# Performance work log

Hardware: AMD Instinct MI355X
Metric: run time of the kernel (lower is better)

## Reference

```python
import jax, jax.numpy as jnp
import numpy as np
from jax import lax

B, L, E = 2, 2048, 1024          # batch, seq_len, embed_dim
NL = 2                            # n_layers
DI = 2 * E                        # d_inner (expand=2)
DS = 16                           # d_state
DC = 4                            # d_conv
DTR = (E + 15) // 16              # dt_rank = ceil(d_model/16) = 64


def setup_inputs() -> dict:
    key = jax.random.key(0)
    ks = jax.random.split(key, 12)
    s = 0.02
    inp = {
        "x": jax.random.normal(ks[0], (B, L, E), jnp.float32),
        "pos_embed": jax.random.normal(ks[1], (L, E), jnp.float32) * s,
        "in_proj_w": jax.random.normal(ks[2], (NL, 2 * DI, E), jnp.float32) * s,
        "conv_w": jax.random.normal(ks[3], (NL, DI, DC), jnp.float32) * s,
        "conv_b": jnp.zeros((NL, DI), jnp.float32),
        "x_proj_w": jax.random.normal(ks[4], (NL, DTR + 2 * DS, DI), jnp.float32) * s,
        "dt_proj_w": jax.random.normal(ks[5], (NL, DI, DTR), jnp.float32) * s,
        "dt_bias": jax.random.normal(ks[6], (NL, DI), jnp.float32) * 0.1,
        "A_log": jnp.broadcast_to(jnp.log(jnp.arange(1, DS + 1, dtype=jnp.float32)), (NL, DI, DS)) + 0.0,
        "D_skip": jnp.ones((NL, DI), jnp.float32),
        "out_proj_w": jax.random.normal(ks[7], (NL, E, DI), jnp.float32) * s,
        "norm_w": jnp.ones((NL, E), jnp.float32),
    }
    return inp


def _rmsnorm(x, w, eps=1e-6):
    return x * lax.rsqrt(jnp.mean(x * x, axis=-1, keepdims=True) + eps) * w


def _mamba(h, in_w, cw, cb, xw, dtw, dtb, A_log, Dp, ow):
    # h: (B, L, E)
    xz = jnp.einsum("ble,de->bld", h, in_w)          # (B, L, 2*DI)
    xc, z = jnp.split(xz, 2, axis=-1)                 # each (B, L, DI)
    # causal depthwise conv1d (kernel DC)
    xp = jnp.pad(xc, ((0, 0), (DC - 1, 0), (0, 0)))
    xconv = cb
    acc = jnp.zeros_like(xc)
    for k in range(DC):
        acc = acc + cw[:, k] * xp[:, k:k + xc.shape[1], :]
    xc = jax.nn.silu(acc + cb)
    # input-dependent SSM params
    x_dbl = jnp.einsum("bld,rd->blr", xc, xw)         # (B, L, DTR+2*DS)
    dt, Bm, C = jnp.split(x_dbl, [DTR, DTR + DS], axis=-1)
    delta = jax.nn.softplus(jnp.einsum("blr,dr->bld", dt, dtw) + dtb)  # (B, L, DI)
    A = -jnp.exp(A_log)                               # (DI, DS)

    def step(hst, inp):
        d, bm, c, u = inp                             # (B,DI),(B,DS),(B,DS),(B,DI)
        hst = jnp.exp(d[..., None] * A) * hst + (d * u)[..., None] * bm[:, None, :]
        y = jnp.einsum("bdn,bn->bd", hst, c)
        return hst, y

    h0 = jnp.zeros((h.shape[0], DI, DS), h.dtype)
    _, ys = lax.scan(step, h0, (delta.swapaxes(0, 1), Bm.swapaxes(0, 1),
                                C.swapaxes(0, 1), xc.swapaxes(0, 1)))
    y = ys.swapaxes(0, 1) + xc * Dp                   # (B, L, DI)
    y = y * jax.nn.silu(z)
    return jnp.einsum("bld,ed->ble", y, ow)


def reference(x, pos_embed, in_proj_w, conv_w, conv_b, x_proj_w, dt_proj_w,
              dt_bias, A_log, D_skip, out_proj_w, norm_w):
    h = x + pos_embed[None, :x.shape[1]]
    for i in range(in_proj_w.shape[0]):
        y = _mamba(h, in_proj_w[i], conv_w[i], conv_b[i], x_proj_w[i],
                   dt_proj_w[i], dt_bias[i], A_log[i], D_skip[i], out_proj_w[i])
        h = _rmsnorm(y + h, norm_w[i])
    return h
```

## Files before the change

### kernel.cpp

```cpp
#include <hip/hip_runtime.h>

#define B_   2
#define L_   2048
#define E_   1024
#define NL_  2
#define DI_  2048
#define DS_  16
#define DC_  4
#define DTR_ 64
#define NXD_ 96
#define M_   (B_ * L_)
#define NCH_ 64
#define LC_  32

typedef __attribute__((ext_vector_type(8))) short bf16x8;
typedef __attribute__((ext_vector_type(4))) float f32x4;

__device__ __forceinline__ float bf2f(unsigned short u) {
    return __uint_as_float(((unsigned)u) << 16);
}
__device__ __forceinline__ unsigned short f2bf(float f) {
    unsigned u = __float_as_uint(f);
    u += 0x7fff + ((u >> 16) & 1);
    return (unsigned short)(u >> 16);
}

#define LOG2E_ 1.44269504f
#define LN2_   0.69314718f

__device__ __forceinline__ float sigmoidf_(float x) {
    return __builtin_amdgcn_rcpf(1.f + __builtin_amdgcn_exp2f(-x * LOG2E_));
}
__device__ __forceinline__ float softplusf_(float x) {
    float e = __builtin_amdgcn_exp2f(x * LOG2E_);
    float s = LN2_ * __builtin_amdgcn_logf(1.f + e);
    return x > 15.f ? x : s;
}
__device__ __forceinline__ float expf_(float x) {
    return __builtin_amdgcn_exp2f(x * LOG2E_);
}
__device__ __forceinline__ float ldin(const void* p, size_t i, int isbf) {
    return isbf ? bf2f(((const unsigned short*)p)[i]) : ((const float*)p)[i];
}
__device__ __forceinline__ void gld_lds16(const unsigned short* g, unsigned short* l) {
    __builtin_amdgcn_global_load_lds(
        (const __attribute__((address_space(1))) unsigned int*)g,
        (__attribute__((address_space(3))) unsigned int*)l, 16, 0, 0);
}
__device__ __forceinline__ bf16x8 ds_read128_(unsigned byteoff) {
    bf16x8 r;
    asm volatile("ds_read_b128 %0, %1" : "=&v"(r) : "v"(byteoff));
    return r;
}

__device__ __forceinline__ void expvec(int fast, float dv, const float* a2, float* e) {
    if (fast) {
        float p1 = __builtin_amdgcn_exp2f(dv * a2[0]);
        float p2 = p1 * p1, p4 = p2 * p2, p8 = p4 * p4;
        e[0] = p1;        e[1] = p2;        e[2] = p2 * p1;   e[3] = p4;
        e[4] = p4 * p1;   e[5] = p4 * p2;   e[6] = e[5] * p1; e[7] = p8;
        e[8] = p8 * p1;   e[9] = p8 * p2;   e[10] = e[9] * p1; e[11] = p8 * p4;
        e[12] = e[11] * p1; e[13] = e[11] * p2; e[14] = e[13] * p1; e[15] = p8 * p8;
    } else {
#pragma unroll
        for (int n = 0; n < 16; ++n) e[n] = __builtin_amdgcn_exp2f(dv * a2[n]);
    }
}

__global__ __launch_bounds__(256) void detect_kernel(const unsigned* __restrict__ x,
                                                     int* __restrict__ flags)
{
    __shared__ int cnt;
    if (threadIdx.x == 0) cnt = 0;
    __syncthreads();
    unsigned v = x[threadIdx.x];
    int e = (v >> 7) & 0xFF;
    if (e >= 90 && e <= 140) atomicAdd(&cnt, 1);
    __syncthreads();
    if (threadIdx.x == 0) {
        flags[0] = (cnt >= 192) ? 1 : 0;
        flags[1] = 1;
        flags[2] = 1;
    }
}

__global__ __launch_bounds__(256) void chk_alog(
    const void* __restrict__ alog, int* __restrict__ flags)
{
    int isbf = flags[0];
    int i = blockIdx.x * 256 + threadIdx.x;
    int layer = i / (DI_ * DS_);
    int n = i & (DS_ - 1);
    float a  = -expf_(ldin(alog, i, isbf));
    float a0 = -expf_(ldin(alog, i - n, isbf));
    float want = (n + 1) * a0;
    if (fabsf(a - want) > 0.02f * fabsf(want))
        atomicAnd(&flags[1 + layer], 0);
}

#define WB_IN_  0
#define WB_XW_  4194304
#define WB_DTW_ 4456448
#define WB_OW_  4587520
#define WB_TOT_ 6684672
__global__ __launch_bounds__(256) void cvt_layer_kernel(
    const void* __restrict__ inw, const void* __restrict__ xw,
    const void* __restrict__ dtw, const void* __restrict__ ow,
    int layer, unsigned short* __restrict__ wbuf, const int* __restrict__ flag)
{
    int isbf = *flag;
    int i = blockIdx.x * 256 + threadIdx.x;
    if (isbf && (i < WB_XW_ || i >= WB_DTW_)) return;
    unsigned short v;
    if (i < WB_XW_) {
        v = isbf ? ((const unsigned short*)inw)[(size_t)layer * 2 * DI_ * E_ + i]
                 : f2bf(((const float*)inw)[(size_t)layer * 2 * DI_ * E_ + i]);
    } else if (i < WB_DTW_) {
        int j = i - WB_XW_; int r = j >> 11, k = j & (DI_ - 1);
        v = (r < NXD_)
          ? (isbf ? ((const unsigned short*)xw)[(size_t)layer * NXD_ * DI_ + (size_t)r * DI_ + k]
                  : f2bf(((const float*)xw)[(size_t)layer * NXD_ * DI_ + (size_t)r * DI_ + k]))
          : (unsigned short)0;
    } else if (i < WB_OW_) {
        int j = i - WB_DTW_;
        v = isbf ? ((const unsigned short*)dtw)[(size_t)layer * DI_ * DTR_ + j]
                 : f2bf(((const float*)dtw)[(size_t)layer * DI_ * DTR_ + j]);
    } else {
        int j = i - WB_OW_;
        v = isbf ? ((const unsigned short*)ow)[(size_t)layer * E_ * DI_ + j]
                 : f2bf(((const float*)ow)[(size_t)layer * E_ * DI_ + j]);
    }
    wbuf[i] = v;
}

__global__ __launch_bounds__(256) void add_pos_kernel(
    const void* __restrict__ x, const void* __restrict__ pos,
    float* __restrict__ h, unsigned short* __restrict__ h16,
    const int* __restrict__ flag)
{
    int isbf = *flag;
    int i = blockIdx.x * 256 + threadIdx.x;
    float v = ldin(x, i, isbf) + ldin(pos, i & (L_ * E_ - 1), isbf);
    h[i] = v;
    h16[i] = f2bf(v);
}

__global__ __launch_bounds__(256) void gemm_mfma(
    const unsigned short* __restrict__ A, int lda,
    const unsigned short* __restrict__ W, int ldw,
    void* __restrict__ C, int ldc, int Ksplit, size_t cSliceStride,
    const void* __restrict__ bias, size_t boff,
    void* __restrict__ C2, int ep, const int* __restrict__ flag,
    const unsigned short* __restrict__ Worig)
{
    __shared__ unsigned short As[128 * 64];
    __shared__ unsigned short Bs[128 * 64];
    int isbf = flag ? *flag : 1;
    const unsigned short* Wp = (Worig && isbf) ? Worig : W;
    int tid = threadIdx.x;
    int lane = tid & 63, w = tid >> 6;
    int m0 = blockIdx.x * 128, n0 = blockIdx.y * 128;
    int wm = (w >> 1) * 64, wn = (w & 1) * 64;
    int col = lane & 15, quad = lane >> 4;
    int kstart = blockIdx.z * Ksplit;

    f32x4 acc[4][4];
#pragma unroll
    for (int i = 0; i < 4; ++i)
#pragma unroll
        for (int j = 0; j < 4; ++j)
            acc[i][j] = (f32x4){0.f, 0.f, 0.f, 0.f};

    for (int kt = kstart; kt < kstart + Ksplit; kt += 64) {
#pragma unroll
        for (int i = 0; i < 4; ++i) {
            int seg = i * 4 + w;
            int q = seg * 64 + lane;
            int r = q >> 3, cd = q & 7;
            int cs = cd ^ (r & 7);
            gld_lds16(A + (size_t)(m0 + r) * lda + kt + cs * 8, &As[seg * 512]);
            gld_lds16(Wp + (size_t)(n0 + r) * ldw + kt + cs * 8, &Bs[seg * 512]);
        }
        __syncthreads();
#pragma unroll
        for (int ks = 0; ks < 2; ++ks) {
            bf16x8 af[4], bfr[4];
#pragma unroll
            for (int t = 0; t < 4; ++t) {
                int rowA = wm + t * 16 + col;
                int ca = ks * 4 + quad;
                af[t]  = *(const bf16x8*)&As[rowA * 64 + ((ca ^ (rowA & 7)) * 8)];
                int rowB = wn + t * 16 + col;
                bfr[t] = *(const bf16x8*)&Bs[rowB * 64 + ((ca ^ (rowB & 7)) * 8)];
            }
#pragma unroll
            for (int tm = 0; tm < 4; ++tm)
#pragma unroll
                for (int tn = 0; tn < 4; ++tn)
                    acc[tm][tn] = __builtin_amdgcn_mfma_f32_16x16x32_bf16(
                        af[tm], bfr[tn], acc[tm][tn], 0, 0, 0);
        }
        __syncthreads();
    }

    float* Cp = (float*)C + (size_t)blockIdx.z * cSliceStride;
#pragma unroll
    for (int tm = 0; tm < 4; ++tm)
#pragma unroll
        for (int tn = 0; tn < 4; ++tn)
#pragma unroll
            for (int rg = 0; rg < 4; ++rg) {
                int gm = m0 + wm + tm * 16 + quad * 4 + rg;
                int gn = n0 + wn + tn * 16 + col;
                float v = acc[tm][tn][rg];
                if (ep == 0) {
                    Cp[(size_t)gm * ldc + gn] = v;
                } else {
                    v = softplusf_(v + ldin(bias, boff + gn, isbf));
                    ((unsigned short*)C)[(size_t)gm * ldc + gn] = f2bf(v);
                }
            }
}

template <int KS, int MH, int RB, int CHK>
__device__ __forceinline__ void g8_phase(
    unsigned baseA, unsigned baseB,
    bf16x8 (&af)[4], bf16x8 (&bfr)[4], f32x4 (&acc)[8][4],
    int doStage, int st_t, int st_isB, int st_ks,
    const unsigned short* srcA, const unsigned short* srcW,
    unsigned short* ldsb, int w)
{
    if (RB) {
#pragma unroll
        for (int j = 0; j < 4; ++j)
            bfr[j] = ds_read128_(baseB + j * 2048 + KS * 1024);
    }
#pragma unroll
    for (int f = 0; f < 4; ++f)
        af[f] = ds_read128_(baseA + MH * 8192 + f * 2048 + KS * 1024);
    if (doStage) {
        const unsigned short* s0 = (st_isB ? srcW : srcA)
            + (size_t)w * 16 * E_ + st_t * 64 + st_ks * 32;
        unsigned short* d0 = ldsb + (st_t & 1) * 32768 + st_isB * 16384
            + w * 1024 + st_ks * 512;
        gld_lds16(s0, d0);
        gld_lds16(s0 + (size_t)8 * 16 * E_, d0 + 8 * 1024);
    }
    __builtin_amdgcn_s_barrier();
    asm volatile("s_waitcnt lgkmcnt(0)" ::: "memory");
    __builtin_amdgcn_sched_barrier(0);
    __builtin_amdgcn_s_setprio(1);
#pragma unroll
    for (int f = 0; f < 4; ++f)
#pragma unroll
        for (int j = 0; j < 4; ++j)
            acc[MH * 4 + f][j] = __builtin_amdgcn_mfma_f32_16x16x32_bf16(
                af[f], bfr[j], acc[MH * 4 + f][j], 0, 0, 0);
    __builtin_amdgcn_s_setprio(0);
    if (CHK == 8) { asm volatile("s_waitcnt vmcnt(8)" ::: "memory"); __builtin_amdgcn_sched_barrier(0); }
    if (CHK == 4) { asm volatile("s_waitcnt vmcnt(4)" ::: "memory"); __builtin_amdgcn_sched_barrier(0); }
    if (CHK == 0) { asm volatile("s_waitcnt vmcnt(0)"  ::: "memory"); __builtin_amdgcn_sched_barrier(0); }
    __builtin_amdgcn_s_barrier();
}

__global__ __launch_bounds__(512) void gemm_inproj8(
    const unsigned short* __restrict__ A,
    const unsigned short* __restrict__ Wbuf,
    const unsigned short* __restrict__ Worig,
    const int* __restrict__ flag,
    unsigned short* __restrict__ Cx,
    unsigned short* __restrict__ Cz)
{
    __shared__ unsigned short lds[65536];
    const unsigned short* W = (*flag) ? Worig : Wbuf;
    int tid = threadIdx.x;
    int lane = tid & 63, w = tid >> 6;
    int wr = w >> 2, wc = w & 3;
    int col = lane & 15, quad = lane >> 4;

    int flat = blockIdx.y * 16 + blockIdx.x;
    int nn = (flat & 7) * 32 + (flat >> 3);
    int cch = nn >> 5, wi = nn & 31;
    int bx = (cch & 3) * 4 + (wi & 3);
    int by = (cch >> 2) * 8 + (wi >> 2);
    int m0 = bx * 256, n0 = by * 256;

    const unsigned short* srcA = A + (size_t)(m0 + (lane & 15)) * E_ + (lane >> 4) * 8;
    const unsigned short* srcW = W + (size_t)(n0 + (lane & 15)) * E_ + (lane >> 4) * 8;

    unsigned baseA0 = (unsigned)(wr * 8 * 2048 + quad * 256 + col * 16);
    unsigned baseB0 = (unsigned)(32768 + wc * 4 * 2048 + quad * 256 + col * 16);
    unsigned baseA1 = baseA0 + 65536, baseB1 = baseB0 + 65536;

    f32x4 acc[8][4];
#pragma unroll
    for (int i = 0; i < 8; ++i)
#pragma unroll
        for (int j = 0; j < 4; ++j)
            acc[i][j] = (f32x4){0.f, 0.f, 0.f, 0.f};
    bf16x8 af[4], bfr[4];

#define G8STAGE(t_, isB_, ks_) { \
    const unsigned short* s0 = ((isB_) ? srcW : srcA) + (size_t)w * 16 * E_ + (t_) * 64 + (ks_) * 32; \
    unsigned short* d0 = lds + ((t_) & 1) * 32768 + (isB_) * 16384 + w * 1024 + (ks_) * 512; \
    gld_lds16(s0, d0); gld_lds16(s0 + (size_t)8 * 16 * E_, d0 + 8 * 1024); }

    G8STAGE(0, 0, 0) G8STAGE(0, 1, 0) G8STAGE(0, 0, 1) G8STAGE(0, 1, 1)
    G8STAGE(1, 0, 0) G8STAGE(1, 1, 0)
    asm volatile("s_waitcnt vmcnt(8)" ::: "memory");
    __builtin_amdgcn_sched_barrier(0);
    __builtin_amdgcn_s_barrier();

    for (int i = 0; i < 7; ++i) {
        int t1 = 2 * i + 1, t2 = 2 * i + 2, t3 = 2 * i + 3;
        g8_phase<0,0,1,-1>(baseA0, baseB0, af, bfr, acc, 1, t1, 0, 1, srcA, srcW, lds, w);
        g8_phase<0,1,0, 8>(baseA0, baseB0, af, bfr, acc, 1, t1, 1, 1, srcA, srcW, lds, w);
        g8_phase<1,0,1,-1>(baseA0, baseB0, af, bfr, acc, 1, t2, 0, 0, srcA, srcW, lds, w);
        g8_phase<1,1,0, 8>(baseA0, baseB0, af, bfr, acc, 1, t2, 1, 0, srcA, srcW, lds, w);
        g8_phase<0,0,1,-1>(baseA1, baseB1, af, bfr, acc, 1, t2, 0, 1, srcA, srcW, lds, w);
        g8_phase<0,1,0, 8>(baseA1, baseB1, af, bfr, acc, 1, t2, 1, 1, srcA, srcW, lds, w);
        g8_phase<1,0,1,-1>(baseA1, baseB1, af, bfr, acc, 1, t3, 0, 0, srcA, srcW, lds, w);
        g8_phase<1,1,0, 8>(baseA1, baseB1, af, bfr, acc, 1, t3, 1, 0, srcA, srcW, lds, w);
    }
    g8_phase<0,0,1,-1>(baseA0, baseB0, af, bfr, acc, 1, 15, 0, 1, srcA, srcW, lds, w);
    g8_phase<0,1,0, 8>(baseA0, baseB0, af, bfr, acc, 1, 15, 1, 1, srcA, srcW, lds, w);
    g8_phase<1,0,1,-1>(baseA0, baseB0, af, bfr, acc, 0, 0, 0, 0, srcA, srcW, lds, w);
    g8_phase<1,1,0, 4>(baseA0, baseB0, af, bfr, acc, 0, 0, 0, 0, srcA, srcW, lds, w);
    g8_phase<0,0,1,-1>(baseA1, baseB1, af, bfr, acc, 0, 0, 0, 0, srcA, srcW, lds, w);
    g8_phase<0,1,0, 0>(baseA1, baseB1, af, bfr, acc, 0, 0, 0, 0, srcA, srcW, lds, w);
    g8_phase<1,0,1,-1>(baseA1, baseB1, af, bfr, acc, 0, 0, 0, 0, srcA, srcW, lds, w);
    g8_phase<1,1,0,-1>(baseA1, baseB1, af, bfr, acc, 0, 0, 0, 0, srcA, srcW, lds, w);

    unsigned short* dst = (n0 < DI_) ? Cx : Cz;
    int nb = (n0 < DI_) ? n0 : n0 - DI_;
#pragma unroll
    for (int tm = 0; tm < 8; ++tm)
#pragma unroll
        for (int tn = 0; tn < 4; ++tn)
#pragma unroll
            for (int rg = 0; rg < 4; ++rg) {
                int gm = m0 + wr * 128 + tm * 16 + quad * 4 + rg;
                int gn = nb + wc * 64 + tn * 16 + col;
                dst[(size_t)gm * DI_ + gn] = f2bf(acc[tm][tn][rg]);
            }
#undef G8STAGE
}

__global__ __launch_bounds__(256) void xproj_reduce(
    const float* __restrict__ part, float* __restrict__ xdbl,
    unsigned short* __restrict__ dt16)
{
    int i = blockIdx.x * 256 + threadIdx.x;
    int r = i >> 7, c = i & 127;
    float v = 0.f;
#pragma unroll
    for (int s = 0; s < 8; ++s) v += part[(size_t)s * (M_ * 128) + i];
    if (c < NXD_) xdbl[(size_t)r * NXD_ + c] = v;
    if (c < DTR_) dt16[(size_t)r * DTR_ + c] = f2bf(v);
}

__global__ __launch_bounds__(256) void conv_prep(
    const void* __restrict__ cw, size_t cwoff, const void* __restrict__ cb,
    size_t cboff, float* __restrict__ cwT, float* __restrict__ cbF,
    const int* __restrict__ flag)
{
    int isbf = *flag;
    int d = blockIdx.x * 256 + threadIdx.x;
#pragma unroll
    for (int k = 0; k < DC_; ++k)
        cwT[k * DI_ + d] = ldin(cw, cwoff + (size_t)d * DC_ + k, isbf);
    cbF[d] = ldin(cb, cboff + d, isbf);
}

#define CT_ 4
__global__ __launch_bounds__(256) void conv_silu_v(
    const unsigned short* __restrict__ xcr16, const float* __restrict__ cwT,
    const float* __restrict__ cbF, unsigned short* __restrict__ xc16)
{
    int g = blockIdx.x;
    int bl0 = g * CT_;
    int l0 = bl0 & (L_ - 1);
    int d = threadIdx.x * 8;

    float w[DC_][8], bias[8];
#pragma unroll
    for (int k = 0; k < DC_; ++k) {
        *(float4*)&w[k][0] = *(const float4*)&cwT[k * DI_ + d];
        *(float4*)&w[k][4] = *(const float4*)&cwT[k * DI_ + d + 4];
    }
    *(float4*)&bias[0] = *(const float4*)&cbF[d];
    *(float4*)&bias[4] = *(const float4*)&cbF[d + 4];

    float xr[DC_ - 1 + CT_][8];
#pragma unroll
    for (int r = 0; r < DC_ - 1 + CT_; ++r) {
        int l = l0 - (DC_ - 1) + r;
        if (l >= 0) {
            bf16x8 v = *(const bf16x8*)&xcr16[(size_t)(bl0 - (DC_ - 1) + r) * DI_ + d];
#pragma unroll
            for (int j = 0; j < 8; ++j) xr[r][j] = bf2f((unsigned short)v[j]);
        } else {
#pragma unroll
            for (int j = 0; j < 8; ++j) xr[r][j] = 0.f;
        }
    }

#pragma unroll
    for (int t = 0; t < CT_; ++t) {
        float acc[8];
#pragma unroll
        for (int j = 0; j < 8; ++j) acc[j] = bias[j];
#pragma unroll
        for (int k = 0; k < DC_; ++k)
#pragma unroll
            for (int j = 0; j < 8; ++j)
                acc[j] = fmaf(w[k][j], xr[t + k][j], acc[j]);
        bf16x8 ov;
#pragma unroll
        for (int j = 0; j < 8; ++j) {
            float s = acc[j] * sigmoidf_(acc[j]);
            ov[j] = (short)f2bf(s);
        }
        *(bf16x8*)&xc16[(size_t)(bl0 + t) * DI_ + d] = ov;
    }
}

__global__ __launch_bounds__(256) void scan_part1(
    const unsigned short* __restrict__ dl16, const unsigned short* __restrict__ xc16,
    const float* __restrict__ xdbl,
    const void* __restrict__ A_log, size_t aoff,
    float* __restrict__ sumdbuf, float* __restrict__ scrS,
    const int* __restrict__ flags, int layer)
{
    int isbf = flags[0], fast = flags[1 + layer];
    __shared__ float bs[LC_][16];
    int c = blockIdx.y;
    int b = blockIdx.x >> 3;
    int d = ((blockIdx.x & 7) << 8) + threadIdx.x;
    for (int i = threadIdx.x; i < LC_ * 16; i += 256) {
        int l = i >> 4, n = i & 15;
        bs[l][n] = xdbl[((size_t)b * L_ + c * LC_ + l) * NXD_ + DTR_ + n];
    }
    __syncthreads();
    float a2[16];
#pragma unroll
    for (int n = 0; n < 16; ++n)
        a2[n] = -expf_(ldin(A_log, aoff + (size_t)d * DS_ + n, isbf)) * LOG2E_;
    float s[16] = {};
    float sumd = 0.f;
    const unsigned short* dp = dl16 + ((size_t)b * L_ + c * LC_) * DI_ + d;
    const unsigned short* up = xc16 + ((size_t)b * L_ + c * LC_) * DI_ + d;
    for (int l0 = 0; l0 < LC_; l0 += 4) {
        float dvv[4], uv[4];
#pragma unroll
        for (int q = 0; q < 4; ++q) {
            dvv[q] = bf2f(dp[(size_t)(l0 + q) * DI_]);
            uv[q]  = bf2f(up[(size_t)(l0 + q) * DI_]);
        }
#pragma unroll
        for (int q = 0; q < 4; ++q) {
            int l = l0 + q;
            float dv = dvv[q];
            sumd += dv;
            float dvu = dv * uv[q];
            float e[16];
            expvec(fast, dv, a2, e);
            float4 b0 = *(const float4*)&bs[l][0];
            float4 b1 = *(const float4*)&bs[l][4];
            float4 b2 = *(const float4*)&bs[l][8];
            float4 b3 = *(const float4*)&bs[l][12];
            float bv[16] = {b0.x,b0.y,b0.z,b0.w, b1.x,b1.y,b1.z,b1.w,
                            b2.x,b2.y,b2.z,b2.w, b3.x,b3.y,b3.z,b3.w};
#pragma unroll
            for (int n = 0; n < 16; ++n)
                s[n] = fmaf(e[n], s[n], dvu * bv[n]);
        }
    }
    int g = b * DI_ + d;
    sumdbuf[(size_t)c * (B_ * DI_) + g] = sumd;
    size_t base = ((size_t)c * (B_ * DI_) + g) * 16;
#pragma unroll
    for (int q = 0; q < 4; ++q)
        *(float4*)&scrS[base + q * 4] =
            make_float4(s[q*4], s[q*4+1], s[q*4+2], s[q*4+3]);
}

__global__ __launch_bounds__(256) void scan_combine(
    const float* __restrict__ sumdbuf, float* __restrict__ scrS,
    const void* __restrict__ A_log, size_t aoff, const int* __restrict__ flags)
{
    int isbf = flags[0];
    int t = blockIdx.x * 256 + threadIdx.x;
    int g = t >> 4, n = t & 15;
    int d = g & (DI_ - 1);
    float a2 = -expf_(ldin(A_log, aoff + (size_t)d * DS_ + n, isbf)) * LOG2E_;
    float sd[NCH_], sl[NCH_];
#pragma unroll
    for (int c = 0; c < NCH_; ++c) {
        sd[c] = sumdbuf[(size_t)c * (B_ * DI_) + g];
        sl[c] = scrS[(size_t)c * (B_ * DI_ * 16) + t];
    }
    float s = 0.f;
#pragma unroll
    for (int c = 0; c < NCH_; ++c) {
        float P = __builtin_amdgcn_exp2f(a2 * sd[c]);
        float nxt = fmaf(P, s, sl[c]);
        scrS[(size_t)c * (B_ * DI_ * 16) + t] = s;
        s = nxt;
    }
}

__global__ __launch_bounds__(256) void scan_part2(
    const unsigned short* __restrict__ dl16, unsigned short* __restrict__ xc16,
    const float* __restrict__ xdbl, const unsigned short* __restrict__ z,
    const void* __restrict__ A_log, size_t aoff,
    const void* __restrict__ Dskip, size_t doff,
    const float* __restrict__ scrS, const int* __restrict__ flags, int layer)
{
    int isbf = flags[0], fast = flags[1 + layer];
    __shared__ float bs[LC_][32];
    int c = blockIdx.y;
    int b = blockIdx.x >> 3;
    int d = ((blockIdx.x & 7) << 8) + threadIdx.x;
    for (int i = threadIdx.x; i < LC_ * 32; i += 256) {
        int l = i >> 5, n = i & 31;
        bs[l][n] = xdbl[((size_t)b * L_ + c * LC_ + l) * NXD_ + DTR_ + n];
    }
    __syncthreads();
    float a2[16];
#pragma unroll
    for (int n = 0; n < 16; ++n)
        a2[n] = -expf_(ldin(A_log, aoff + (size_t)d * DS_ + n, isbf)) * LOG2E_;
    float Dv = ldin(Dskip, doff + d, isbf);
    int g = b * DI_ + d;
    size_t sbase = ((size_t)c * (B_ * DI_) + g) * 16;
    float s[16];
#pragma unroll
    for (int q = 0; q < 4; ++q) {
        float4 sv = *(const float4*)&scrS[sbase + q * 4];
        s[q*4] = sv.x; s[q*4+1] = sv.y; s[q*4+2] = sv.z; s[q*4+3] = sv.w;
    }

    const unsigned short* dp = dl16 + ((size_t)b * L_ + c * LC_) * DI_ + d;
    unsigned short* up = xc16 + ((size_t)b * L_ + c * LC_) * DI_ + d;
    const unsigned short* zp = z + ((size_t)b * L_ + c * LC_) * DI_ + d;
    for (int l0 = 0; l0 < LC_; l0 += 4) {
        float dvv[4], uv[4], zv[4];
#pragma unroll
        for (int q = 0; q < 4; ++q) {
            dvv[q] = bf2f(dp[(size_t)(l0 + q) * DI_]);
            uv[q]  = bf2f(up[(size_t)(l0 + q) * DI_]);
            zv[q]  = bf2f(zp[(size_t)(l0 + q) * DI_]);
        }
#pragma unroll
        for (int q = 0; q < 4; ++q) {
            int l = l0 + q;
            float dv = dvv[q], u = uv[q];
            float dvu = dv * u;
            float e[16];
            expvec(fast, dv, a2, e);
            float4 b0 = *(const float4*)&bs[l][0];
            float4 b1 = *(const float4*)&bs[l][4];
            float4 b2 = *(const float4*)&bs[l][8];
            float4 b3 = *(const float4*)&bs[l][12];
            float4 c0 = *(const float4*)&bs[l][16];
            float4 c1 = *(const float4*)&bs[l][20];
            float4 c2 = *(const float4*)&bs[l][24];
            float4 c3 = *(const float4*)&bs[l][28];
            float bv[16] = {b0.x,b0.y,b0.z,b0.w, b1.x,b1.y,b1.z,b1.w,
                            b2.x,b2.y,b2.z,b2.w, b3.x,b3.y,b3.z,b3.w};
            float cv[16] = {c0.x,c0.y,c0.z,c0.w, c1.x,c1.y,c1.z,c1.w,
                            c2.x,c2.y,c2.z,c2.w, c3.x,c3.y,c3.z,c3.w};
            float y = 0.f;
#pragma unroll
            for (int n = 0; n < 16; ++n) {
                s[n] = fmaf(e[n], s[n], dvu * bv[n]);
                y = fmaf(s[n], cv[n], y);
            }
            float zvv = zv[q];
            up[(size_t)l * DI_] = f2bf((y + u * Dv) * (zvv * sigmoidf_(zvv)));
        }
    }
}

__global__ __launch_bounds__(256) void rmsnorm_kernel(
    const float* __restrict__ y0, const float* __restrict__ y1,
    float* __restrict__ h, unsigned short* __restrict__ h16,
    const void* __restrict__ nw, size_t nwoff, void* __restrict__ out,
    int write_out, const int* __restrict__ flag)
{
    int isbf = *flag;
    __shared__ float red[4];
    int row = blockIdx.x;
    float* hp = h + (size_t)row * E_;
    float v[4]; float ss = 0.f;
#pragma unroll
    for (int i = 0; i < 4; ++i) {
        int e = threadIdx.x + i * 256;
        size_t idx = (size_t)row * E_ + e;
        v[i] = y0[idx] + y1[idx] + hp[e];
        ss += v[i] * v[i];
    }
#pragma unroll
    for (int off = 1; off < 64; off <<= 1) ss += __shfl_xor(ss, off, 64);
    if ((threadIdx.x & 63) == 0) red[threadIdx.x >> 6] = ss;
    __syncthreads();
    ss = red[0] + red[1] + red[2] + red[3];
    float scale = rsqrtf(ss * (1.f / E_) + 1e-6f);
#pragma unroll
    for (int i = 0; i < 4; ++i) {
        int e = threadIdx.x + i * 256;
        float hv = v[i] * scale * ldin(nw, nwoff + e, isbf);
        hp[e] = hv;
        h16[(size_t)row * E_ + e] = f2bf(hv);
        if (write_out) {
            size_t oi = (size_t)row * E_ + e;
            if (isbf) ((unsigned short*)out)[oi] = f2bf(hv);
            else      ((float*)out)[oi] = hv;
        }
    }
}

extern "C" void kernel_launch(void* const* d_in, const int* in_sizes, int n_in,
                              void* d_out, int out_size, void* d_ws, size_t ws_size,
                              hipStream_t stream)
{
    const void* x    = d_in[0];
    const void* pos  = d_in[1];
    const void* inw  = d_in[2];
    const void* cw   = d_in[3];
    const void* cb   = d_in[4];
    const void* xw   = d_in[5];
    const void* dtw  = d_in[6];
    const void* dtb  = d_in[7];
    const void* alog = d_in[8];
    const void* dsk  = d_in[9];
    const void* ow   = d_in[10];
    const void* nw   = d_in[11];

    float* ws = (float*)d_ws;
    float* h      = ws;
    unsigned short* h16  = (unsigned short*)(ws + 4194304);
    unsigned short* z16  = (unsigned short*)(ws + 6291456);
    unsigned short* xc16 = (unsigned short*)(ws + 10485760);
    float* D      = ws + 14680064;
    float* R      = ws + 23068672;
    float* xdbl   = ws + 27262976;
    unsigned short* dt16 = (unsigned short*)(ws + 27656192);
    float* sumd   = ws + 27787264;
    unsigned short* wbuf = (unsigned short*)(ws + 28049408);
    int* flags    = (int*)(ws + 31391744);

    unsigned short* xcr16 = (unsigned short*)R;
    float* xp_part = R;
    float* scrS    = R;
    unsigned short* dl16 = (unsigned short*)D;
    float* yout0 = D;
    float* yout1 = D + (size_t)M_ * E_;
    float* cwT = sumd;
    float* cbF = sumd + DC_ * DI_;

    detect_kernel<<<1, 256, 0, stream>>>((const unsigned*)x, flags);
    chk_alog<<<NL_ * DI_ * DS_ / 256, 256, 0, stream>>>(alog, flags);
    add_pos_kernel<<<M_ * E_ / 256, 256, 0, stream>>>(x, pos, h, h16, flags);

    for (int layer = 0; layer < NL_; ++layer) {
        const unsigned short* inws = (const unsigned short*)inw + (size_t)layer * 2 * DI_ * E_;
        const unsigned short* dtws = (const unsigned short*)dtw + (size_t)layer * DI_ * DTR_;
        const unsigned short* ows  = (const unsigned short*)ow  + (size_t)layer * E_ * DI_;

        cvt_layer_kernel<<<WB_TOT_ / 256, 256, 0, stream>>>(
            inw, xw, dtw, ow, layer, wbuf, flags);
        conv_prep<<<DI_ / 256, 256, 0, stream>>>(
            cw, (size_t)layer * DI_ * DC_, cb, (size_t)layer * DI_, cwT, cbF, flags);

        gemm_inproj8<<<dim3(M_ / 256, 2 * DI_ / 256, 1), 512, 0, stream>>>(
            h16, wbuf + WB_IN_, inws, flags, xcr16, z16);
        conv_silu_v<<<M_ / CT_, 256, 0, stream>>>(xcr16, cwT, cbF, xc16);
        gemm_mfma<<<dim3(M_ / 128, 1, 8), 256, 0, stream>>>(
            xc16, DI_, wbuf + WB_XW_, DI_, xp_part, 128, DI_ / 8, (size_t)M_ * 128,
            nullptr, 0, nullptr, 0, flags, nullptr);
        xproj_reduce<<<M_ * 128 / 256, 256, 0, stream>>>(xp_part, xdbl, dt16);
        gemm_mfma<<<dim3(M_ / 128, DI_ / 128, 1), 256, 0, stream>>>(
            dt16, DTR_, wbuf + WB_DTW_, DTR_, dl16, DI_, DTR_, 0,
            dtb, (size_t)layer * DI_, nullptr, 2, flags, dtws);
        scan_part1<<<dim3(B_ * DI_ / 256, NCH_), 256, 0, stream>>>(
            dl16, xc16, xdbl, alog, (size_t)layer * DI_ * DS_, sumd, scrS, flags, layer);
        scan_combine<<<B_ * DI_ * DS_ / 256, 256, 0, stream>>>(
            sumd, scrS, alog, (size_t)layer * DI_ * DS_, flags);
        scan_part2<<<dim3(B_ * DI_ / 256, NCH_), 256, 0, stream>>>(
            dl16, xc16, xdbl, z16, alog, (size_t)layer * DI_ * DS_,
            dsk, (size_t)layer * DI_, scrS, flags, layer);
        gemm_mfma<<<dim3(M_ / 128, E_ / 128, 2), 256, 0, stream>>>(
            xc16, DI_, wbuf + WB_OW_, DI_, yout0, E_, DI_ / 2, (size_t)M_ * E_,
            nullptr, 0, nullptr, 0, flags, ows);
        rmsnorm_kernel<<<M_, 256, 0, stream>>>(
            yout0, yout1, h, h16, nw, (size_t)layer * E_, d_out,
            layer == NL_ - 1 ? 1 : 0, flags);
    }
}
```

Before: 553.0 us.

## Software-pipeline scan loads, merge conv prep into cvt kernel, widen add_pos

Both scan passes now double-buffer their per-timestep loads of delta, u and z, issuing the next group of four loads before computing the current group. The goal is to hide global-memory latency in these serial recurrences. The conv weight and bias prep moves into the first blocks of the weight-conversion kernel, which saves one launch per layer. add_pos now does four elements per thread with a quarter of the blocks. Holding two load buffers adds register pressure in the scan kernels.

New measurement: 1.134 ms. 2.05x slower.

```diff
diff --git a/kernel.cpp b/kernel.cpp
--- a/kernel.cpp
+++ b/kernel.cpp
@@ -106,9 +106,18 @@
 __global__ __launch_bounds__(256) void cvt_layer_kernel(
     const void* __restrict__ inw, const void* __restrict__ xw,
     const void* __restrict__ dtw, const void* __restrict__ ow,
-    int layer, unsigned short* __restrict__ wbuf, const int* __restrict__ flag)
+    int layer, unsigned short* __restrict__ wbuf, const int* __restrict__ flag,
+    const void* __restrict__ cw, size_t cwoff, const void* __restrict__ cb,
+    size_t cboff, float* __restrict__ cwT, float* __restrict__ cbF)
 {
     int isbf = *flag;
+    if (blockIdx.x < DI_ / 256) {
+        int d = blockIdx.x * 256 + threadIdx.x;
+#pragma unroll
+        for (int k = 0; k < DC_; ++k)
+            cwT[k * DI_ + d] = ldin(cw, cwoff + (size_t)d * DC_ + k, isbf);
+        cbF[d] = ldin(cb, cboff + d, isbf);
+    }
     int i = blockIdx.x * 256 + threadIdx.x;
     if (isbf && (i < WB_XW_ || i >= WB_DTW_)) return;
     unsigned short v;
@@ -139,10 +148,14 @@
     const int* __restrict__ flag)
 {
     int isbf = *flag;
-    int i = blockIdx.x * 256 + threadIdx.x;
-    float v = ldin(x, i, isbf) + ldin(pos, i & (L_ * E_ - 1), isbf);
-    h[i] = v;
-    h16[i] = f2bf(v);
+    int i4 = (blockIdx.x * 256 + threadIdx.x) * 4;
+#pragma unroll
+    for (int q = 0; q < 4; ++q) {
+        int i = i4 + q;
+        float v = ldin(x, i, isbf) + ldin(pos, i & (L_ * E_ - 1), isbf);
+        h[i] = v;
+        h16[i] = f2bf(v);
+    }
 }
 
 __global__ __launch_bounds__(256) void gemm_mfma(
@@ -359,19 +372,6 @@
     if (c < DTR_) dt16[(size_t)r * DTR_ + c] = f2bf(v);
 }
 
-__global__ __launch_bounds__(256) void conv_prep(
-    const void* __restrict__ cw, size_t cwoff, const void* __restrict__ cb,
-    size_t cboff, float* __restrict__ cwT, float* __restrict__ cbF,
-    const int* __restrict__ flag)
-{
-    int isbf = *flag;
-    int d = blockIdx.x * 256 + threadIdx.x;
-#pragma unroll
-    for (int k = 0; k < DC_; ++k)
-        cwT[k * DI_ + d] = ldin(cw, cwoff + (size_t)d * DC_ + k, isbf);
-    cbF[d] = ldin(cb, cboff + d, isbf);
-}
-
 #define CT_ 4
 __global__ __launch_bounds__(256) void conv_silu_v(
     const unsigned short* __restrict__ xcr16, const float* __restrict__ cwT,
@@ -422,6 +422,84 @@
             ov[j] = (short)f2bf(s);
         }
         *(bf16x8*)&xc16[(size_t)(bl0 + t) * DI_ + d] = ov;
+    }
+}
+
+__device__ __forceinline__ void scan_ld2(const unsigned short* dp,
+    const unsigned short* up, int l0, float (&dvv)[4], float (&uv)[4])
+{
+#pragma unroll
+    for (int q = 0; q < 4; ++q) {
+        dvv[q] = bf2f(dp[(size_t)(l0 + q) * DI_]);
+        uv[q]  = bf2f(up[(size_t)(l0 + q) * DI_]);
+    }
+}
+__device__ __forceinline__ void scan_ld3(const unsigned short* dp,
+    const unsigned short* up, const unsigned short* zp, int l0,
+    float (&dvv)[4], float (&uv)[4], float (&zv)[4])
+{
+#pragma unroll
+    for (int q = 0; q < 4; ++q) {
+        dvv[q] = bf2f(dp[(size_t)(l0 + q) * DI_]);
+        uv[q]  = bf2f(up[(size_t)(l0 + q) * DI_]);
+        zv[q]  = bf2f(zp[(size_t)(l0 + q) * DI_]);
+    }
+}
+__device__ __forceinline__ void scan1_grp(int fast, const float* a2,
+    float (&s)[16], float& sumd, const float (&dvv)[4], const float (&uv)[4],
+    const float (*bs)[16], int l0)
+{
+#pragma unroll
+    for (int q = 0; q < 4; ++q) {
+        int l = l0 + q;
+        float dv = dvv[q];
+        sumd += dv;
+        float dvu = dv * uv[q];
+        float e[16];
+        expvec(fast, dv, a2, e);
+        float4 b0 = *(const float4*)&bs[l][0];
+        float4 b1 = *(const float4*)&bs[l][4];
+        float4 b2 = *(const float4*)&bs[l][8];
+        float4 b3 = *(const float4*)&bs[l][12];
+        float bv[16] = {b0.x,b0.y,b0.z,b0.w, b1.x,b1.y,b1.z,b1.w,
+                        b2.x,b2.y,b2.z,b2.w, b3.x,b3.y,b3.z,b3.w};
+#pragma unroll
+        for (int n = 0; n < 16; ++n)
+            s[n] = fmaf(e[n], s[n], dvu * bv[n]);
+    }
+}
+__device__ __forceinline__ void scan2_grp(int fast, const float* a2,
+    float (&s)[16], float Dv, const float (&dvv)[4], const float (&uv)[4],
+    const float (&zv)[4], const float (*bs)[32], int l0,
+    unsigned short* up)
+{
+#pragma unroll
+    for (int q = 0; q < 4; ++q) {
+        int l = l0 + q;
+        float dv = dvv[q], u = uv[q];
+        float dvu = dv * u;
+        float e[16];
+        expvec(fast, dv, a2, e);
+        float4 b0 = *(const float4*)&bs[l][0];
+        float4 b1 = *(const float4*)&bs[l][4];
+        float4 b2 = *(const float4*)&bs[l][8];
+        float4 b3 = *(const float4*)&bs[l][12];
+        float4 c0 = *(const float4*)&bs[l][16];
+        float4 c1 = *(const float4*)&bs[l][20];
+        float4 c2 = *(const float4*)&bs[l][24];
+        float4 c3 = *(const float4*)&bs[l][28];
+        float bv[16] = {b0.x,b0.y,b0.z,b0.w, b1.x,b1.y,b1.z,b1.w,
+                        b2.x,b2.y,b2.z,b2.w, b3.x,b3.y,b3.z,b3.w};
+        float cv[16] = {c0.x,c0.y,c0.z,c0.w, c1.x,c1.y,c1.z,c1.w,
+                        c2.x,c2.y,c2.z,c2.w, c3.x,c3.y,c3.z,c3.w};
+        float y = 0.f;
+#pragma unroll
+        for (int n = 0; n < 16; ++n) {
+            s[n] = fmaf(e[n], s[n], dvu * bv[n]);
+            y = fmaf(s[n], cv[n], y);
+        }
+        float zvv = zv[q];
+        up[(size_t)l * DI_] = f2bf((y + u * Dv) * (zvv * sigmoidf_(zvv)));
     }
 }
 
@@ -450,32 +528,20 @@
     float sumd = 0.f;
     const unsigned short* dp = dl16 + ((size_t)b * L_ + c * LC_) * DI_ + d;
     const unsigned short* up = xc16 + ((size_t)b * L_ + c * LC_) * DI_ + d;
-    for (int l0 = 0; l0 < LC_; l0 += 4) {
-        float dvv[4], uv[4];
-#pragma unroll
-        for (int q = 0; q < 4; ++q) {
-            dvv[q] = bf2f(dp[(size_t)(l0 + q) * DI_]);
-            uv[q]  = bf2f(up[(size_t)(l0 + q) * DI_]);
-        }
-#pragma unroll
-        for (int q = 0; q < 4; ++q) {
-            int l = l0 + q;
-            float dv = dvv[q];
-            sumd += dv;
-            float dvu = dv * uv[q];
-            float e[16];
-            expvec(fast, dv, a2, e);
-            float4 b0 = *(const float4*)&bs[l][0];
-            float4 b1 = *(const float4*)&bs[l][4];
-            float4 b2 = *(const float4*)&bs[l][8];
-            float4 b3 = *(const float4*)&bs[l][12];
-            float bv[16] = {b0.x,b0.y,b0.z,b0.w, b1.x,b1.y,b1.z,b1.w,
-                            b2.x,b2.y,b2.z,b2.w, b3.x,b3.y,b3.z,b3.w};
-#pragma unroll
-            for (int n = 0; n < 16; ++n)
-                s[n] = fmaf(e[n], s[n], dvu * bv[n]);
-        }
-    }
+
+    float dA[4], uA[4], dB[4], uB[4];
+    scan_ld2(dp, up, 0, dA, uA);
+#pragma unroll
+    for (int l0 = 0; l0 < LC_ - 8; l0 += 8) {
+        scan_ld2(dp, up, l0 + 4, dB, uB);
+        scan1_grp(fast, a2, s, sumd, dA, uA, bs, l0);
+        scan_ld2(dp, up, l0 + 8, dA, uA);
+        scan1_grp(fast, a2, s, sumd, dB, uB, bs, l0 + 4);
+    }
+    scan_ld2(dp, up, LC_ - 4, dB, uB);
+    scan1_grp(fast, a2, s, sumd, dA, uA, bs, LC_ - 8);
+    scan1_grp(fast, a2, s, sumd, dB, uB, bs, LC_ - 4);
+
     int g = b * DI_ + d;
     sumdbuf[(size_t)c * (B_ * DI_) + g] = sumd;
     size_t base = ((size_t)c * (B_ * DI_) + g) * 16;
@@ -544,43 +610,19 @@
     const unsigned short* dp = dl16 + ((size_t)b * L_ + c * LC_) * DI_ + d;
     unsigned short* up = xc16 + ((size_t)b * L_ + c * LC_) * DI_ + d;
     const unsigned short* zp = z + ((size_t)b * L_ + c * LC_) * DI_ + d;
-    for (int l0 = 0; l0 < LC_; l0 += 4) {
-        float dvv[4], uv[4], zv[4];
-#pragma unroll
-        for (int q = 0; q < 4; ++q) {
-            dvv[q] = bf2f(dp[(size_t)(l0 + q) * DI_]);
-            uv[q]  = bf2f(up[(size_t)(l0 + q) * DI_]);
-            zv[q]  = bf2f(zp[(size_t)(l0 + q) * DI_]);
-        }
-#pragma unroll
-        for (int q = 0; q < 4; ++q) {
-            int l = l0 + q;
-            float dv = dvv[q], u = uv[q];
-            float dvu = dv * u;
-            float e[16];
-            expvec(fast, dv, a2, e);
-            float4 b0 = *(const float4*)&bs[l][0];
-            float4 b1 = *(const float4*)&bs[l][4];
-            float4 b2 = *(const float4*)&bs[l][8];
-            float4 b3 = *(const float4*)&bs[l][12];
-            float4 c0 = *(const float4*)&bs[l][16];
-            float4 c1 = *(const float4*)&bs[l][20];
-            float4 c2 = *(const float4*)&bs[l][24];
-            float4 c3 = *(const float4*)&bs[l][28];
-            float bv[16] = {b0.x,b0.y,b0.z,b0.w, b1.x,b1.y,b1.z,b1.w,
-                            b2.x,b2.y,b2.z,b2.w, b3.x,b3.y,b3.z,b3.w};
-            float cv[16] = {c0.x,c0.y,c0.z,c0.w, c1.x,c1.y,c1.z,c1.w,
-                            c2.x,c2.y,c2.z,c2.w, c3.x,c3.y,c3.z,c3.w};
-            float y = 0.f;
-#pragma unroll
-            for (int n = 0; n < 16; ++n) {
-                s[n] = fmaf(e[n], s[n], dvu * bv[n]);
-                y = fmaf(s[n], cv[n], y);
-            }
-            float zvv = zv[q];
-            up[(size_t)l * DI_] = f2bf((y + u * Dv) * (zvv * sigmoidf_(zvv)));
-        }
-    }
+
+    float dA[4], uA[4], zA[4], dB[4], uB[4], zB[4];
+    scan_ld3(dp, up, zp, 0, dA, uA, zA);
+#pragma unroll
+    for (int l0 = 0; l0 < LC_ - 8; l0 += 8) {
+        scan_ld3(dp, up, zp, l0 + 4, dB, uB, zB);
+        scan2_grp(fast, a2, s, Dv, dA, uA, zA, bs, l0, up);
+        scan_ld3(dp, up, zp, l0 + 8, dA, uA, zA);
+        scan2_grp(fast, a2, s, Dv, dB, uB, zB, bs, l0 + 4, up);
+    }
+    scan_ld3(dp, up, zp, LC_ - 4, dB, uB, zB);
+    scan2_grp(fast, a2, s, Dv, dA, uA, zA, bs, LC_ - 8, up);
+    scan2_grp(fast, a2, s, Dv, dB, uB, zB, bs, LC_ - 4, up);
 }
 
 __global__ __launch_bounds__(256) void rmsnorm_kernel(
@@ -662,7 +704,7 @@
 
     detect_kernel<<<1, 256, 0, stream>>>((const unsigned*)x, flags);
     chk_alog<<<NL_ * DI_ * DS_ / 256, 256, 0, stream>>>(alog, flags);
-    add_pos_kernel<<<M_ * E_ / 256, 256, 0, stream>>>(x, pos, h, h16, flags);
+    add_pos_kernel<<<M_ * E_ / 1024, 256, 0, stream>>>(x, pos, h, h16, flags);
 
     for (int layer = 0; layer < NL_; ++layer) {
         const unsigned short* inws = (const unsigned short*)inw + (size_t)layer * 2 * DI_ * E_;
@@ -670,9 +712,8 @@
         const unsigned short* ows  = (const unsigned short*)ow  + (size_t)layer * E_ * DI_;
 
         cvt_layer_kernel<<<WB_TOT_ / 256, 256, 0, stream>>>(
-            inw, xw, dtw, ow, layer, wbuf, flags);
-        conv_prep<<<DI_ / 256, 256, 0, stream>>>(
-            cw, (size_t)layer * DI_ * DC_, cb, (size_t)layer * DI_, cwT, cbF, flags);
+            inw, xw, dtw, ow, layer, wbuf, flags,
+            cw, (size_t)layer * DI_ * DC_, cb, (size_t)layer * DI_, cwT, cbF);
 
         gemm_inproj8<<<dim3(M_ / 256, 2 * DI_ / 256, 1), 512, 0, stream>>>(
             h16, wbuf + WB_IN_, inws, flags, xcr16, z16);
```
